# Kernel tuning notes

Hardware: AMD Instinct MI355X
Metric: run time of the kernel (lower is better)

The kernel has to match this reference:

```python
import jax, jax.numpy as jnp
import numpy as np

S, K, N, G = 4096, 64, 4096, 512
P = S * K
DIST_BINS = np.array([1, 2, 3, 4, 8, 16, 32, 64], dtype=np.int64)  # 10-bucket distance embedding
PAD_VALUE = 1000.0


def setup_inputs() -> dict:
    key = jax.random.key(0)
    ks = jax.random.split(key, 15)
    return {
        "g_i": jax.random.normal(ks[0], (N, G), dtype=jnp.float32),
        "mention_scores": jax.random.normal(ks[1], (N, 1), dtype=jnp.float32),
        "dist_embed": jax.random.normal(ks[2], (10, 20), dtype=jnp.float32),
        "genre_embed": jax.random.normal(ks[3], (7, 20), dtype=jnp.float32),
        "speaker_embed": jax.random.normal(ks[4], (3, 20), dtype=jnp.float32),
        "W1": jax.random.normal(ks[5], (3 * G + 60, 150), dtype=jnp.float32) * 0.02,
        "b1": jax.random.normal(ks[6], (150,), dtype=jnp.float32) * 0.02,
        "W2": jax.random.normal(ks[7], (150, 1), dtype=jnp.float32) * 0.02,
        "b2": jax.random.normal(ks[8], (1,), dtype=jnp.float32) * 0.02,
        "mention_ids": jax.random.randint(ks[9], (P,), 0, N, dtype=jnp.int64),
        "antecedent_ids": jax.random.randint(ks[10], (P,), 0, N, dtype=jnp.int64),
        "distances": jax.random.randint(ks[11], (P,), 0, 300, dtype=jnp.int64),
        "genres": jax.random.randint(ks[12], (P,), 0, 7, dtype=jnp.int64),
        "speakers": jax.random.randint(ks[13], (P,), 0, 3, dtype=jnp.int64),
        "ant_counts": jax.random.randint(ks[14], (S,), 0, K, dtype=jnp.int64),
    }


def reference(g_i, mention_scores, dist_embed, genre_embed, speaker_embed,
              W1, b1, W2, b2,
              mention_ids, antecedent_ids, distances, genres, speakers, ant_counts):
    # --- phi: distance / genre / speaker embeddings, [P, 60] ---
    buckets = jnp.sum(distances[:, None] >= jnp.asarray(DIST_BINS), axis=1)  # [P] in [0, 8]
    phi = jnp.concatenate(
        [dist_embed[buckets], genre_embed[genres], speaker_embed[speakers]], axis=1)

    # --- pairwise features: (g_i, g_j, g_i * g_j, phi), [P, 3G+60] ---
    i_g = g_i[mention_ids]
    j_g = g_i[antecedent_ids]
    pairs = jnp.concatenate([i_g, j_g, i_g * j_g, phi], axis=1)

    # --- Score MLP: Linear -> ReLU -> Linear, [P, 1] ---
    h = jax.nn.relu(pairs @ W1 + b1)
    s_ij = h @ W2 + b2

    # --- coref score: s_i + s_j + s_ij ---
    coref = mention_scores[mention_ids] + mention_scores[antecedent_ids] + s_ij  # [P, 1]
    scores = coref.reshape(S, K)

    # --- per-span softmax over valid antecedents + epsilon (dummy) column ---
    valid = jnp.arange(K)[None, :] < ant_counts[:, None]            # [S, K]
    logits = jnp.where(valid, scores, -1e9)
    logits = jnp.concatenate([logits, jnp.zeros((S, 1), logits.dtype)], axis=1)  # epsilon = 0
    probs = jax.nn.softmax(logits, axis=1)                          # [S, K+1]

    # pad_and_stack(value=1000): overwrite invalid slots with pad value
    valid_eps = jnp.concatenate([valid, jnp.ones((S, 1), dtype=bool)], axis=1)
    probs = jnp.where(valid_eps, probs, PAD_VALUE)
    return probs
```

## Files before the change

kernel.cpp:

```cpp
#include <hip/hip_runtime.h>

#define NMENT 4096
#define GDIM  512
#define NPAD  160
#define NOUT  150

typedef _Float16 f16x8 __attribute__((ext_vector_type(8)));
typedef float    f32x4 __attribute__((ext_vector_type(4)));
typedef float    f32x2 __attribute__((ext_vector_type(2)));

#if defined(__has_builtin)
#if __has_builtin(__builtin_amdgcn_cvt_pk_f32_fp8) && __has_builtin(__builtin_amdgcn_cvt_pk_fp8_f32)
#define FP8_HW 1
#endif
#endif

__device__ __forceinline__ float fp8_dec1f(unsigned b) {
    unsigned em = b & 0x7fu;
    unsigned bits = (em < 8u) ? 0u : (((b & 0x80u) << 24) | ((em + 960u) << 20));
    return __builtin_bit_cast(float, bits);
}
__device__ __forceinline__ unsigned fp8_enc1f(float x) {
    float c = fminf(fmaxf(x, -448.f), 448.f);
    unsigned u = __builtin_bit_cast(unsigned, c);
    unsigned s = (u >> 24) & 0x80u;
    unsigned mag = (u & 0x7fffffffu) + 0x80000u;
    int em = (int)(mag >> 20) - 960;
    if (em <= 0) return s;
    if (em > 0x7e) em = 0x7e;
    return s | (unsigned)em;
}
__device__ __forceinline__ f32x2 fp8_dec2_lo(unsigned v) {
#ifdef FP8_HW
    return __builtin_amdgcn_cvt_pk_f32_fp8((int)v, false);
#else
    f32x2 r; r[0] = fp8_dec1f(v & 0xffu); r[1] = fp8_dec1f((v >> 8) & 0xffu); return r;
#endif
}
__device__ __forceinline__ f32x2 fp8_dec2_hi(unsigned v) {
#ifdef FP8_HW
    return __builtin_amdgcn_cvt_pk_f32_fp8((int)v, true);
#else
    f32x2 r; r[0] = fp8_dec1f((v >> 16) & 0xffu); r[1] = fp8_dec1f(v >> 24); return r;
#endif
}
__device__ __forceinline__ unsigned fp8_enc1(float x) {
#ifdef FP8_HW
    return (unsigned)__builtin_amdgcn_cvt_pk_fp8_f32(x, x, 0, false) & 0xffu;
#else
    return fp8_enc1f(x);
#endif
}
__device__ __forceinline__ unsigned fp8_pack4(float a, float b, float c, float d) {
#ifdef FP8_HW
    int v = __builtin_amdgcn_cvt_pk_fp8_f32(a, b, 0, false);
    v = __builtin_amdgcn_cvt_pk_fp8_f32(c, d, v, true);
    return (unsigned)v;
#else
    return fp8_enc1f(a) | (fp8_enc1f(b) << 8) | (fp8_enc1f(c) << 16) | (fp8_enc1f(d) << 24);
#endif
}
__device__ __forceinline__ uint2 fp8_mul8_fp8(uint2 a, uint2 b) {
    f32x2 a0 = fp8_dec2_lo(a.x), a1 = fp8_dec2_hi(a.x);
    f32x2 a2 = fp8_dec2_lo(a.y), a3 = fp8_dec2_hi(a.y);
    f32x2 b0 = fp8_dec2_lo(b.x), b1 = fp8_dec2_hi(b.x);
    f32x2 b2 = fp8_dec2_lo(b.y), b3 = fp8_dec2_hi(b.y);
    f32x2 p0 = a0 * b0, p1 = a1 * b1, p2 = a2 * b2, p3 = a3 * b3;
    uint2 r;
    r.x = fp8_pack4(p0[0], p0[1], p1[0], p1[1]);
    r.y = fp8_pack4(p2[0], p2[1], p3[0], p3[1]);
    return r;
}
__device__ __forceinline__ f16x8 fp8_to_f16x8(uint2 a) {
    f32x2 a0 = fp8_dec2_lo(a.x), a1 = fp8_dec2_hi(a.x);
    f32x2 a2 = fp8_dec2_lo(a.y), a3 = fp8_dec2_hi(a.y);
    uint4 r;
    r.x = __builtin_bit_cast(unsigned, __builtin_amdgcn_cvt_pkrtz(a0[0], a0[1]));
    r.y = __builtin_bit_cast(unsigned, __builtin_amdgcn_cvt_pkrtz(a1[0], a1[1]));
    r.z = __builtin_bit_cast(unsigned, __builtin_amdgcn_cvt_pkrtz(a2[0], a2[1]));
    r.w = __builtin_bit_cast(unsigned, __builtin_amdgcn_cvt_pkrtz(a3[0], a3[1]));
    return __builtin_bit_cast(f16x8, r);
}

#define G8_OFF    0u
#define WT_OFF    2097152u
#define WC8_OFF   2588672u
#define NODEI_OFF 2670592u
#define NODEJ_OFF 3325952u
#define PHI_OFF   3981312u
#define B1P_OFF   4014912u
#define W2P_OFF   4015552u

__global__ void prep_kernel(const float* __restrict__ g_i,
                            const float* __restrict__ de,
                            const float* __restrict__ ge,
                            const float* __restrict__ se,
                            const float* __restrict__ W1,
                            const float* __restrict__ b1,
                            const float* __restrict__ W2,
                            unsigned char* __restrict__ g8,
                            _Float16* __restrict__ WT,
                            unsigned char* __restrict__ Wc8,
                            unsigned char* __restrict__ Phi8,
                            float* __restrict__ b1p,
                            float* __restrict__ W2p)
{
    __shared__ float tl[64 * 152];
    const int b = blockIdx.x, tid = threadIdx.x;

    if (b < 1024) {
        const float4* g4 = (const float4*)g_i;
        int i4 = b * 512 + tid * 2;
        float4 v0 = g4[i4], v1 = g4[i4 + 1];
        unsigned lo = fp8_pack4(v0.x, v0.y, v0.z, v0.w);
        unsigned hi = fp8_pack4(v1.x, v1.y, v1.z, v1.w);
        ((uint2*)g8)[b * 256 + tid] = make_uint2(lo, hi);
    } else if (b < 1048) {
        int b2 = b - 1024, j = b2 >> 3, k0 = (b2 & 7) << 6;
        int rbase = j * 512 + k0;
        for (int idx = tid; idx < 64 * 150; idx += 256) {
            int kk = idx / 150, col = idx - kk * 150;
            tl[kk * 152 + col] = W1[(rbase + kk) * 150 + col];
        }
        __syncthreads();
        for (int idx = tid; idx < 160 * 64; idx += 256) {
            int n = idx >> 6, k = idx & 63;
            float v = (n < 150) ? tl[k * 152 + n] : 0.0f;
            if (j < 2) {
                WT[j * 81920 + n * 512 + k0 + k] = (_Float16)v;
            } else {
                int t = n >> 4, c16 = n & 15;
                int kg = k0 + k;
                int ks = kg >> 5, quad = (kg >> 3) & 3, jj = kg & 7;
                Wc8[(t * 16 + ks) * 512 + (c16 * 4 + quad) * 8 + jj]
                    = (unsigned char)fp8_enc1(v);
            }
        }
    } else if (b < 1180) {
        int e = (b - 1048) * 256 + tid;
        if (e < 210 * 160) {
            int c = e / 160, n = e - c * 160;
            float acc = 0.0f;
            if (n < 150) {
                int bk = c / 21, rest = c - bk * 21, gi = rest / 3, sp = rest - gi * 3;
                #pragma unroll 4
                for (int d = 0; d < 20; ++d) {
                    acc += de[bk * 20 + d] * W1[(1536 + d) * 150 + n];
                    acc += ge[gi * 20 + d] * W1[(1556 + d) * 150 + n];
                    acc += se[sp * 20 + d] * W1[(1576 + d) * 150 + n];
                }
            }
            Phi8[e] = (unsigned char)fp8_enc1(acc);
        }
    } else if (b == 1180) {
        if (tid < 160) b1p[tid] = (tid < 150) ? b1[tid] : 0.0f;
    } else {
        if (tid < 160) W2p[tid] = (tid < 150) ? W2[tid] : 0.0f;
    }
}

__global__ __launch_bounds__(256) void p1_node(
    const unsigned char* __restrict__ g8,
    const _Float16* __restrict__ WT,
    const float* __restrict__ b1p,
    unsigned char* __restrict__ NodeI8,
    unsigned char* __restrict__ NodeJ8)
{
    const int tid = threadIdx.x, y = blockIdx.y;
    const int lane = tid & 63, w = tid >> 6;
    const int col = lane & 15, quad = lane >> 4;
    const int mhalf = w >> 1, nhalf = w & 1;
    const int rowbase = blockIdx.x * 64 + mhalf * 32;

    const uint2* a0p = (const uint2*)(g8 + (rowbase + col) * 512) + quad;
    const uint2* a1p = (const uint2*)(g8 + (rowbase + 16 + col) * 512) + quad;
    const uint4* B = (const uint4*)(WT + y * 81920);
    unsigned char* outp = y ? NodeJ8 : NodeI8;

    const uint4* bp[5];
    #pragma unroll
    for (int t = 0; t < 5; ++t)
        bp[t] = B + (nhalf * 80 + t * 16 + col) * 64 + quad;

    f32x4 acc[2][5];
    #pragma unroll
    for (int mt = 0; mt < 2; ++mt)
        #pragma unroll
        for (int t = 0; t < 5; ++t) acc[mt][t] = f32x4{0.f, 0.f, 0.f, 0.f};

    #pragma unroll 2
    for (int ks = 0; ks < 16; ++ks) {
        f16x8 a0 = fp8_to_f16x8(a0p[ks * 4]);
        f16x8 a1 = fp8_to_f16x8(a1p[ks * 4]);
        #pragma unroll
        for (int t = 0; t < 5; ++t) {
            f16x8 bf = __builtin_bit_cast(f16x8, bp[t][ks * 4]);
            acc[0][t] = __builtin_amdgcn_mfma_f32_16x16x32_f16(a0, bf, acc[0][t], 0, 0, 0);
            acc[1][t] = __builtin_amdgcn_mfma_f32_16x16x32_f16(a1, bf, acc[1][t], 0, 0, 0);
        }
    }

    #pragma unroll
    for (int mt = 0; mt < 2; ++mt)
        #pragma unroll
        for (int t = 0; t < 5; ++t) {
            int n = nhalf * 80 + t * 16 + col;
            float bias = y ? 0.0f : b1p[n];
            #pragma unroll
            for (int r = 0; r < 4; ++r) {
                int row = rowbase + mt * 16 + quad * 4 + r;
                outp[row * NPAD + n] = (unsigned char)fp8_enc1(acc[mt][t][r] + bias);
            }
        }
}

__global__ __launch_bounds__(256, 3) void pair_score_kernel(
    const unsigned char* __restrict__ g8,
    const unsigned char* __restrict__ Wc8,
    const unsigned char* __restrict__ NodeI8,
    const unsigned char* __restrict__ NodeJ8,
    const unsigned char* __restrict__ Phi8,
    const float* __restrict__ W2p,
    const float* __restrict__ msc,
    const float* __restrict__ b2,
    const int* __restrict__ mention_ids,
    const int* __restrict__ ant_ids,
    const int* __restrict__ dists,
    const int* __restrict__ genres,
    const int* __restrict__ speakers,
    const int* __restrict__ ant_counts,
    float* __restrict__ out)
{
    __shared__ __align__(16) unsigned char smem[64 * 164 * 4];
    __shared__ int   m_lds[64], a_lds[64];
    __shared__ float sc[64];

    const int tid = threadIdx.x, s = blockIdx.x;
    const int lane = tid & 63;
    const int col = lane & 15, quad = lane >> 4;

    if (tid < 64) {
        int p = s * 64 + tid;
        m_lds[tid] = mention_ids[p];
        a_lds[tid] = ant_ids[p];
    }
    __syncthreads();

    #pragma unroll 4
    for (int c = tid; c < 64 * 64; c += 256) {
        int row = c >> 6, ko = (c & 63) * 8;
        uint2 gi = *(const uint2*)(g8 + m_lds[row] * 512 + ko);
        uint2 gj = *(const uint2*)(g8 + a_lds[row] * 512 + ko);
        *(uint2*)&smem[row * 528 + ko] = fp8_mul8_fp8(gi, gj);
    }
    __syncthreads();

    const int wS = __builtin_amdgcn_readfirstlane(tid >> 6);
    const int base = (wS < 2) ? wS * 3 : 6 + (wS - 2) * 2;
    const int cnt  = (wS < 2) ? 3 : 2;
    const int laneoff = (col * 4 + quad) * 8;

    f32x4 acc[4][3];
    #pragma unroll
    for (int mt = 0; mt < 4; ++mt)
        #pragma unroll
        for (int tt = 0; tt < 3; ++tt) acc[mt][tt] = f32x4{0.f, 0.f, 0.f, 0.f};

    const unsigned char* bbase = Wc8 + base * 16 * 512 + laneoff;

    #pragma unroll 4
    for (int ks = 0; ks < 16; ++ks) {
        long av[4];
        #pragma unroll
        for (int mt = 0; mt < 4; ++mt)
            av[mt] = *(const long*)&smem[(mt * 16 + col) * 528 + ks * 32 + quad * 8];
        #pragma unroll
        for (int tt = 0; tt < 3; ++tt) {
            if (tt < cnt) {
                long bv = *(const long*)(bbase + (tt * 16 + ks) * 512);
                #pragma unroll
                for (int mt = 0; mt < 4; ++mt)
                    acc[mt][tt] = __builtin_amdgcn_mfma_f32_16x16x32_fp8_fp8(
                        av[mt], bv, acc[mt][tt], 0, 0, 0);
            }
        }
    }
    __syncthreads();

    float* CLDS = (float*)smem;
    #pragma unroll
    for (int tt = 0; tt < 3; ++tt) {
        if (tt < cnt) {
            #pragma unroll
            for (int mt = 0; mt < 4; ++mt)
                #pragma unroll
                for (int r = 0; r < 4; ++r)
                    CLDS[(mt * 16 + quad * 4 + r) * 164 + (base + tt) * 16 + col]
                        = acc[mt][tt][r];
        }
    }
    __syncthreads();

    const int pe = tid >> 2, q = tid & 3;
    const int pp = s * 64 + pe;
    const int me = m_lds[pe], ae = a_lds[pe];
    const int d = dists[pp];
    const int bk = (d>=1)+(d>=2)+(d>=3)+(d>=4)+(d>=8)+(d>=16)+(d>=32)+(d>=64);
    const int ce = (bk * 7 + genres[pp]) * 3 + speakers[pp];

    const unsigned* NI = (const unsigned*)(NodeI8 + me * NPAD) + q * 10;
    const unsigned* NJ = (const unsigned*)(NodeJ8 + ae * NPAD) + q * 10;
    const unsigned* PH = (const unsigned*)(Phi8 + ce * NPAD) + q * 10;
    const float* crow = &CLDS[pe * 164 + q * 40];
    const float* w2r = W2p + q * 40;

    float sum = 0.0f;
    #pragma unroll
    for (int i = 0; i < 10; ++i) {
        unsigned ni = NI[i], nj = NJ[i], ph = PH[i];
        float4 cf = *(const float4*)(crow + i * 4);
        float4 wf = *(const float4*)(w2r + i * 4);
        f32x2 ni0 = fp8_dec2_lo(ni), ni1 = fp8_dec2_hi(ni);
        f32x2 nj0 = fp8_dec2_lo(nj), nj1 = fp8_dec2_hi(nj);
        f32x2 ph0 = fp8_dec2_lo(ph), ph1 = fp8_dec2_hi(ph);
        sum += fmaxf(cf.x + ni0[0] + nj0[0] + ph0[0], 0.0f) * wf.x;
        sum += fmaxf(cf.y + ni0[1] + nj0[1] + ph0[1], 0.0f) * wf.y;
        sum += fmaxf(cf.z + ni1[0] + nj1[0] + ph1[0], 0.0f) * wf.z;
        sum += fmaxf(cf.w + ni1[1] + nj1[1] + ph1[1], 0.0f) * wf.w;
    }
    sum += __shfl_xor(sum, 1);
    sum += __shfl_xor(sum, 2);
    if (q == 0) sc[pe] = sum;
    __syncthreads();

    if (tid < 64) {
        int cnt2 = ant_counts[s];
        bool valid = tid < cnt2;
        float logit = valid
            ? (sc[tid] + msc[m_lds[tid]] + msc[a_lds[tid]] + b2[0])
            : -1e30f;
        float mx = logit;
        mx = fmaxf(mx, __shfl_xor(mx, 1));  mx = fmaxf(mx, __shfl_xor(mx, 2));
        mx = fmaxf(mx, __shfl_xor(mx, 4));  mx = fmaxf(mx, __shfl_xor(mx, 8));
        mx = fmaxf(mx, __shfl_xor(mx, 16)); mx = fmaxf(mx, __shfl_xor(mx, 32));
        mx = fmaxf(mx, 0.0f);
        float e = __expf(logit - mx);
        float ssum = e;
        ssum += __shfl_xor(ssum, 1);  ssum += __shfl_xor(ssum, 2);
        ssum += __shfl_xor(ssum, 4);  ssum += __shfl_xor(ssum, 8);
        ssum += __shfl_xor(ssum, 16); ssum += __shfl_xor(ssum, 32);
        float eps = __expf(-mx);
        ssum += eps;
        float* orow = out + s * 65;
        orow[tid] = valid ? (e / ssum) : 1000.0f;
        if (tid == 0) orow[64] = eps / ssum;
    }
}

extern "C" void kernel_launch(void* const* d_in, const int* in_sizes, int n_in,
                              void* d_out, int out_size, void* d_ws, size_t ws_size,
                              hipStream_t stream)
{
    const float* g_i = (const float*)d_in[0];
    const float* msc = (const float*)d_in[1];
    const float* de  = (const float*)d_in[2];
    const float* ge  = (const float*)d_in[3];
    const float* se  = (const float*)d_in[4];
    const float* W1  = (const float*)d_in[5];
    const float* b1  = (const float*)d_in[6];
    const float* W2  = (const float*)d_in[7];
    const float* b2  = (const float*)d_in[8];
    const int* mid  = (const int*)d_in[9];
    const int* aid  = (const int*)d_in[10];
    const int* dst  = (const int*)d_in[11];
    const int* gen  = (const int*)d_in[12];
    const int* spk  = (const int*)d_in[13];
    const int* cnts = (const int*)d_in[14];

    char* ws = (char*)d_ws;
    unsigned char* g8    = (unsigned char*)(ws + G8_OFF);
    _Float16*      WT    = (_Float16*)(ws + WT_OFF);
    unsigned char* Wc8   = (unsigned char*)(ws + WC8_OFF);
    unsigned char* NodeI = (unsigned char*)(ws + NODEI_OFF);
    unsigned char* NodeJ = (unsigned char*)(ws + NODEJ_OFF);
    unsigned char* Phi8  = (unsigned char*)(ws + PHI_OFF);
    float*         b1p   = (float*)(ws + B1P_OFF);
    float*         W2p   = (float*)(ws + W2P_OFF);

    prep_kernel<<<dim3(1182), dim3(256), 0, stream>>>(
        g_i, de, ge, se, W1, b1, W2, g8, WT, Wc8, Phi8, b1p, W2p);

    p1_node<<<dim3(64, 2), dim3(256), 0, stream>>>(
        g8, WT, b1p, NodeI, NodeJ);

    pair_score_kernel<<<dim3(4096), dim3(256), 0, stream>>>(
        g8, Wc8, NodeI, NodeJ, Phi8, W2p, msc, b2,
        mid, aid, dst, gen, spk, cnts, (float*)d_out);
}
```

Before: 191.4 us.

## Use FP8 MFMA for node projections and fp16 LDS staging in pair kernel

```diff
diff --git a/kernel.cpp b/kernel.cpp
--- a/kernel.cpp
+++ b/kernel.cpp
@@ -6,6 +6,7 @@
 #define NOUT  150
 
 typedef _Float16 f16x8 __attribute__((ext_vector_type(8)));
+typedef _Float16 f16x4 __attribute__((ext_vector_type(4)));
 typedef float    f32x4 __attribute__((ext_vector_type(4)));
 typedef float    f32x2 __attribute__((ext_vector_type(2)));
 
@@ -71,25 +72,14 @@
     r.y = fp8_pack4(p2[0], p2[1], p3[0], p3[1]);
     return r;
 }
-__device__ __forceinline__ f16x8 fp8_to_f16x8(uint2 a) {
-    f32x2 a0 = fp8_dec2_lo(a.x), a1 = fp8_dec2_hi(a.x);
-    f32x2 a2 = fp8_dec2_lo(a.y), a3 = fp8_dec2_hi(a.y);
-    uint4 r;
-    r.x = __builtin_bit_cast(unsigned, __builtin_amdgcn_cvt_pkrtz(a0[0], a0[1]));
-    r.y = __builtin_bit_cast(unsigned, __builtin_amdgcn_cvt_pkrtz(a1[0], a1[1]));
-    r.z = __builtin_bit_cast(unsigned, __builtin_amdgcn_cvt_pkrtz(a2[0], a2[1]));
-    r.w = __builtin_bit_cast(unsigned, __builtin_amdgcn_cvt_pkrtz(a3[0], a3[1]));
-    return __builtin_bit_cast(f16x8, r);
-}
 
 #define G8_OFF    0u
-#define WT_OFF    2097152u
-#define WC8_OFF   2588672u
-#define NODEI_OFF 2670592u
-#define NODEJ_OFF 3325952u
-#define PHI_OFF   3981312u
-#define B1P_OFF   4014912u
-#define W2P_OFF   4015552u
+#define WABC_OFF  2097152u
+#define NODEI_OFF 2342912u
+#define NODEJ_OFF 2998272u
+#define PHI_OFF   3653632u
+#define B1P_OFF   3687232u
+#define W2P_OFF   3687872u
 
 __global__ void prep_kernel(const float* __restrict__ g_i,
                             const float* __restrict__ de,
@@ -99,8 +89,7 @@
                             const float* __restrict__ b1,
                             const float* __restrict__ W2,
                             unsigned char* __restrict__ g8,
-                            _Float16* __restrict__ WT,
-                            unsigned char* __restrict__ Wc8,
+                            unsigned char* __restrict__ Wabc8,
                             unsigned char* __restrict__ Phi8,
                             float* __restrict__ b1p,
                             float* __restrict__ W2p)
@@ -126,15 +115,11 @@
         for (int idx = tid; idx < 160 * 64; idx += 256) {
             int n = idx >> 6, k = idx & 63;
             float v = (n < 150) ? tl[k * 152 + n] : 0.0f;
-            if (j < 2) {
-                WT[j * 81920 + n * 512 + k0 + k] = (_Float16)v;
-            } else {
-                int t = n >> 4, c16 = n & 15;
-                int kg = k0 + k;
-                int ks = kg >> 5, quad = (kg >> 3) & 3, jj = kg & 7;
-                Wc8[(t * 16 + ks) * 512 + (c16 * 4 + quad) * 8 + jj]
-                    = (unsigned char)fp8_enc1(v);
-            }
+            int tile = j * 10 + (n >> 4), c16 = n & 15;
+            int kg = k0 + k;
+            int ks = kg >> 5, quad = (kg >> 3) & 3, jj = kg & 7;
+            Wabc8[(tile * 16 + ks) * 512 + (c16 * 4 + quad) * 8 + jj]
+                = (unsigned char)fp8_enc1(v);
         }
     } else if (b < 1180) {
         int e = (b - 1048) * 256 + tid;
@@ -159,62 +144,70 @@
     }
 }
 
-__global__ __launch_bounds__(256) void p1_node(
+__global__ __launch_bounds__(256, 2) void p1_node(
     const unsigned char* __restrict__ g8,
-    const _Float16* __restrict__ WT,
+    const unsigned char* __restrict__ Wabc8,
     const float* __restrict__ b1p,
     unsigned char* __restrict__ NodeI8,
     unsigned char* __restrict__ NodeJ8)
 {
-    const int tid = threadIdx.x, y = blockIdx.y;
-    const int lane = tid & 63, w = tid >> 6;
+    __shared__ __align__(16) unsigned char A8s[32 * 528];
+    const int tid = threadIdx.x;
+    const int lane = tid & 63;
     const int col = lane & 15, quad = lane >> 4;
-    const int mhalf = w >> 1, nhalf = w & 1;
-    const int rowbase = blockIdx.x * 64 + mhalf * 32;
-
-    const uint2* a0p = (const uint2*)(g8 + (rowbase + col) * 512) + quad;
-    const uint2* a1p = (const uint2*)(g8 + (rowbase + 16 + col) * 512) + quad;
-    const uint4* B = (const uint4*)(WT + y * 81920);
-    unsigned char* outp = y ? NodeJ8 : NodeI8;
-
-    const uint4* bp[5];
-    #pragma unroll
-    for (int t = 0; t < 5; ++t)
-        bp[t] = B + (nhalf * 80 + t * 16 + col) * 64 + quad;
+    const int rowbase = blockIdx.x * 32;
+
+    #pragma unroll
+    for (int idx = tid; idx < 32 * 32; idx += 256) {
+        int row = idx >> 5, o = (idx & 31) * 16;
+        uint4 v = *(const uint4*)(g8 + (rowbase + row) * 512 + o);
+        *(uint4*)&A8s[row * 528 + o] = v;
+    }
+    __syncthreads();
+
+    const int wS = __builtin_amdgcn_readfirstlane(tid >> 6);
+    const unsigned char* bbase = Wabc8 + (wS * 5 * 16) * 512 + (col * 4 + quad) * 8;
 
     f32x4 acc[2][5];
     #pragma unroll
     for (int mt = 0; mt < 2; ++mt)
         #pragma unroll
-        for (int t = 0; t < 5; ++t) acc[mt][t] = f32x4{0.f, 0.f, 0.f, 0.f};
-
-    #pragma unroll 2
+        for (int tt = 0; tt < 5; ++tt) acc[mt][tt] = f32x4{0.f, 0.f, 0.f, 0.f};
+
+    #pragma unroll 4
     for (int ks = 0; ks < 16; ++ks) {
-        f16x8 a0 = fp8_to_f16x8(a0p[ks * 4]);
-        f16x8 a1 = fp8_to_f16x8(a1p[ks * 4]);
-        #pragma unroll
-        for (int t = 0; t < 5; ++t) {
-            f16x8 bf = __builtin_bit_cast(f16x8, bp[t][ks * 4]);
-            acc[0][t] = __builtin_amdgcn_mfma_f32_16x16x32_f16(a0, bf, acc[0][t], 0, 0, 0);
-            acc[1][t] = __builtin_amdgcn_mfma_f32_16x16x32_f16(a1, bf, acc[1][t], 0, 0, 0);
-        }
-    }
-
-    #pragma unroll
-    for (int mt = 0; mt < 2; ++mt)
-        #pragma unroll
-        for (int t = 0; t < 5; ++t) {
-            int n = nhalf * 80 + t * 16 + col;
-            float bias = y ? 0.0f : b1p[n];
+        long av[2];
+        #pragma unroll
+        for (int mt = 0; mt < 2; ++mt)
+            av[mt] = *(const long*)&A8s[(mt * 16 + col) * 528 + ks * 32 + quad * 8];
+        #pragma unroll
+        for (int tt = 0; tt < 5; ++tt) {
+            long bv = *(const long*)(bbase + (tt * 16 + ks) * 512);
+            #pragma unroll
+            for (int mt = 0; mt < 2; ++mt)
+                acc[mt][tt] = __builtin_amdgcn_mfma_f32_16x16x32_fp8_fp8(
+                    av[mt], bv, acc[mt][tt], 0, 0, 0);
+        }
+    }
+
+    #pragma unroll
+    for (int tt = 0; tt < 5; ++tt) {
+        int tglob = wS * 5 + tt;
+        bool isI = tglob < 10;
+        int n = (isI ? tglob : tglob - 10) * 16 + col;
+        unsigned char* outp = isI ? NodeI8 : NodeJ8;
+        float bias = isI ? b1p[n] : 0.0f;
+        #pragma unroll
+        for (int mt = 0; mt < 2; ++mt)
             #pragma unroll
             for (int r = 0; r < 4; ++r) {
                 int row = rowbase + mt * 16 + quad * 4 + r;
-                outp[row * NPAD + n] = (unsigned char)fp8_enc1(acc[mt][t][r] + bias);
+                outp[row * NPAD + n] = (unsigned char)fp8_enc1(acc[mt][tt][r] + bias);
             }
-        }
-}
-
-__global__ __launch_bounds__(256, 3) void pair_score_kernel(
+    }
+}
+
+__global__ __launch_bounds__(256, 4) void pair_score_kernel(
     const unsigned char* __restrict__ g8,
     const unsigned char* __restrict__ Wc8,
     const unsigned char* __restrict__ NodeI8,
@@ -231,7 +224,7 @@
     const int* __restrict__ ant_counts,
     float* __restrict__ out)
 {
-    __shared__ __align__(16) unsigned char smem[64 * 164 * 4];
+    __shared__ __align__(16) unsigned char smem[64 * 528];
     __shared__ int   m_lds[64], a_lds[64];
     __shared__ float sc[64];
 
@@ -287,7 +280,7 @@
     }
     __syncthreads();
 
-    float* CLDS = (float*)smem;
+    _Float16* CLDS16 = (_Float16*)smem;
     #pragma unroll
     for (int tt = 0; tt < 3; ++tt) {
         if (tt < cnt) {
@@ -295,8 +288,8 @@
             for (int mt = 0; mt < 4; ++mt)
                 #pragma unroll
                 for (int r = 0; r < 4; ++r)
-                    CLDS[(mt * 16 + quad * 4 + r) * 164 + (base + tt) * 16 + col]
-                        = acc[mt][tt][r];
+                    CLDS16[(mt * 16 + quad * 4 + r) * 168 + (base + tt) * 16 + col]
+                        = (_Float16)acc[mt][tt][r];
         }
     }
     __syncthreads();
@@ -311,22 +304,22 @@
     const unsigned* NI = (const unsigned*)(NodeI8 + me * NPAD) + q * 10;
     const unsigned* NJ = (const unsigned*)(NodeJ8 + ae * NPAD) + q * 10;
     const unsigned* PH = (const unsigned*)(Phi8 + ce * NPAD) + q * 10;
-    const float* crow = &CLDS[pe * 164 + q * 40];
+    const _Float16* crow = CLDS16 + pe * 168 + q * 40;
     const float* w2r = W2p + q * 40;
 
     float sum = 0.0f;
     #pragma unroll
     for (int i = 0; i < 10; ++i) {
         unsigned ni = NI[i], nj = NJ[i], ph = PH[i];
-        float4 cf = *(const float4*)(crow + i * 4);
+        f16x4 cf4 = *(const f16x4*)(crow + i * 4);
         float4 wf = *(const float4*)(w2r + i * 4);
         f32x2 ni0 = fp8_dec2_lo(ni), ni1 = fp8_dec2_hi(ni);
         f32x2 nj0 = fp8_dec2_lo(nj), nj1 = fp8_dec2_hi(nj);
         f32x2 ph0 = fp8_dec2_lo(ph), ph1 = fp8_dec2_hi(ph);
-        sum += fmaxf(cf.x + ni0[0] + nj0[0] + ph0[0], 0.0f) * wf.x;
-        sum += fmaxf(cf.y + ni0[1] + nj0[1] + ph0[1], 0.0f) * wf.y;
-        sum += fmaxf(cf.z + ni1[0] + nj1[0] + ph1[0], 0.0f) * wf.z;
-        sum += fmaxf(cf.w + ni1[1] + nj1[1] + ph1[1], 0.0f) * wf.w;
+        sum += fmaxf((float)cf4[0] + ni0[0] + nj0[0] + ph0[0], 0.0f) * wf.x;
+        sum += fmaxf((float)cf4[1] + ni0[1] + nj0[1] + ph0[1], 0.0f) * wf.y;
+        sum += fmaxf((float)cf4[2] + ni1[0] + nj1[0] + ph1[0], 0.0f) * wf.z;
+        sum += fmaxf((float)cf4[3] + ni1[1] + nj1[1] + ph1[1], 0.0f) * wf.w;
     }
     sum += __shfl_xor(sum, 1);
     sum += __shfl_xor(sum, 2);
@@ -379,8 +372,7 @@
 
     char* ws = (char*)d_ws;
     unsigned char* g8    = (unsigned char*)(ws + G8_OFF);
-    _Float16*      WT    = (_Float16*)(ws + WT_OFF);
-    unsigned char* Wc8   = (unsigned char*)(ws + WC8_OFF);
+    unsigned char* Wabc8 = (unsigned char*)(ws + WABC_OFF);
     unsigned char* NodeI = (unsigned char*)(ws + NODEI_OFF);
     unsigned char* NodeJ = (unsigned char*)(ws + NODEJ_OFF);
     unsigned char* Phi8  = (unsigned char*)(ws + PHI_OFF);
@@ -388,12 +380,12 @@
     float*         W2p   = (float*)(ws + W2P_OFF);
 
     prep_kernel<<<dim3(1182), dim3(256), 0, stream>>>(
-        g_i, de, ge, se, W1, b1, W2, g8, WT, Wc8, Phi8, b1p, W2p);
-
-    p1_node<<<dim3(64, 2), dim3(256), 0, stream>>>(
-        g8, WT, b1p, NodeI, NodeJ);
+        g_i, de, ge, se, W1, b1, W2, g8, Wabc8, Phi8, b1p, W2p);
+
+    p1_node<<<dim3(128), dim3(256), 0, stream>>>(
+        g8, Wabc8, b1p, NodeI, NodeJ);
 
     pair_score_kernel<<<dim3(4096), dim3(256), 0, stream>>>(
-        g8, Wc8, NodeI, NodeJ, Phi8, W2p, msc, b2,
+        g8, Wabc8 + 20 * 16 * 512, NodeI, NodeJ, Phi8, W2p, msc, b2,
         mid, aid, dst, gen, spk, cnts, (float*)d_out);
 }
```

New measurement: 170.6 us. 1.12x faster.
